# Performance work log

Measured on AMD Instinct MI355X. Metric: run time of the kernel, lower is better.

Reference implementation:

```python
import jax, jax.numpy as jnp
import numpy as np

EPS = 1e-5
SCALE = 2
K_UP = 5


def _conv(x, w, pad):
    return jax.lax.conv_general_dilated(
        x, w, window_strides=(1, 1), padding=[(pad, pad), (pad, pad)],
        dimension_numbers=("NCHW", "OIHW", "NCHW"))


def _bn(x, gamma, beta, mean, var):
    scale = gamma / jnp.sqrt(var + EPS)
    return x * scale[None, :, None, None] + (beta - mean * scale)[None, :, None, None]


def _pixel_shuffle(x, r):
    b, cr2, h, w = x.shape
    c = cr2 // (r * r)
    x = x.reshape(b, c, r, r, h, w)
    x = x.transpose(0, 1, 4, 2, 5, 3)  # b, c, h, r, w, r
    return x.reshape(b, c, h * r, w * r)


def setup_inputs() -> dict:
    key = jax.random.key(0)
    ks = jax.random.split(key, 6)
    c, c_mid, k_enc = 256, 64, 3
    n_k = (SCALE * K_UP) ** 2  # 100
    return {
        "x": jax.random.normal(ks[0], (2, c, 64, 64), jnp.float32),
        "comp_w": jax.random.normal(ks[1], (c_mid, c, 1, 1), jnp.float32) * 0.05,
        "comp_gamma": jnp.ones((c_mid,), jnp.float32),
        "comp_beta": jnp.zeros((c_mid,), jnp.float32),
        "comp_mean": jax.random.normal(ks[2], (c_mid,), jnp.float32) * 0.1,
        "comp_var": jax.random.uniform(ks[3], (c_mid,), jnp.float32, 0.5, 1.5),
        "enc_w": jax.random.normal(ks[4], (n_k, c_mid, k_enc, k_enc), jnp.float32) * 0.05,
        "enc_gamma": jnp.ones((n_k,), jnp.float32),
        "enc_beta": jnp.zeros((n_k,), jnp.float32),
        "enc_mean": jax.random.normal(ks[5], (n_k,), jnp.float32) * 0.1,
        "enc_var": jnp.ones((n_k,), jnp.float32),
    }


def reference(x, comp_w, comp_gamma, comp_beta, comp_mean, comp_var,
              enc_w, enc_gamma, enc_beta, enc_mean, enc_var):
    b, c, h, w = x.shape
    h_, w_ = h * SCALE, w * SCALE
    # comp: 1x1 conv -> BN -> ReLU
    W = jax.nn.relu(_bn(_conv(x, comp_w, 0), comp_gamma, comp_beta, comp_mean, comp_var))
    # enc: 3x3 conv -> BN (no relu)
    W = _bn(_conv(W, enc_w, 1), enc_gamma, enc_beta, enc_mean, enc_var)
    # pixel shuffle to [b, k_up^2, h_, w_] then softmax over kernel dim
    W = _pixel_shuffle(W, SCALE)
    W = jax.nn.softmax(W, axis=1)
    # nearest upsample x2
    Xu = jnp.repeat(jnp.repeat(x, SCALE, axis=2), SCALE, axis=3)
    # unfold: kernel k_up, dilation=SCALE, padding=k_up//2*SCALE
    pad = (K_UP // 2) * SCALE
    Xp = jnp.pad(Xu, ((0, 0), (0, 0), (pad, pad), (pad, pad)))
    patches = jnp.stack(
        [Xp[:, :, i * SCALE:i * SCALE + h_, j * SCALE:j * SCALE + w_]
         for i in range(K_UP) for j in range(K_UP)], axis=2)  # [b,c,k^2,h_,w_]
    return jnp.einsum("bkhw,bckhw->bchw", W, patches)
```

## Files before the change

### kernel.cpp

```cpp
#include <hip/hip_runtime.h>
#include <hip/hip_bf16.h>

#define EPSF 1e-5f

__global__ void k1_comp(const float* __restrict__ x, const float* __restrict__ w,
                        const float* __restrict__ gamma, const float* __restrict__ beta,
                        const float* __restrict__ mean, const float* __restrict__ var,
                        float* __restrict__ comp) {
    int t = blockIdx.x * 256 + threadIdx.x;
    int p  = t & 4095;
    int mq = (t >> 12) & 15;
    int b  = t >> 16;
    int m0 = mq * 4;
    const float* xb = x + b * (256 * 4096) + p;
    float acc[4] = {0.f, 0.f, 0.f, 0.f};
    #pragma unroll 16
    for (int c = 0; c < 256; ++c) {
        float xv = xb[c << 12];
        #pragma unroll
        for (int m = 0; m < 4; ++m)
            acc[m] += xv * w[(m0 + m) * 256 + c];
    }
    #pragma unroll
    for (int m = 0; m < 4; ++m) {
        int mo = m0 + m;
        float s = gamma[mo] * rsqrtf(var[mo] + EPSF);
        float r = acc[m] * s + (beta[mo] - mean[mo] * s);
        comp[(b * 64 + mo) * 4096 + p] = fmaxf(r, 0.f);
    }
}

__global__ void k2_enc_part(const float* __restrict__ comp, const float* __restrict__ w,
                            float* __restrict__ encp) {
    __shared__ float sh[16 * 18 * 18];
    const int tile = blockIdx.x;
    const int og   = blockIdx.y >> 2;
    const int icc  = blockIdx.y & 3;
    const int b    = blockIdx.z;
    const int ty0 = (tile >> 2) << 4;
    const int tx0 = (tile & 3) << 4;
    const int tid = threadIdx.x;
    const int tx = tid & 15, ty = tid >> 4;
    const int o0 = og * 10;

    const float* cb = comp + b * (64 * 4096);
    for (int idx = tid; idx < 16 * 324; idx += 256) {
        int ic_l = idx / 324;
        int rem  = idx - ic_l * 324;
        int yy = rem / 18;
        int xx = rem - yy * 18;
        int gy = ty0 + yy - 1;
        int gx = tx0 + xx - 1;
        float v = 0.f;
        if (gy >= 0 && gy < 64 && gx >= 0 && gx < 64)
            v = cb[((icc * 16 + ic_l) << 12) + (gy << 6) + gx];
        sh[idx] = v;
    }
    __syncthreads();

    float acc[10];
    #pragma unroll
    for (int i = 0; i < 10; ++i) acc[i] = 0.f;

    #pragma unroll 4
    for (int ic_l = 0; ic_l < 16; ++ic_l) {
        const float* base = sh + ic_l * 324 + ty * 18 + tx;
        float v[9];
        #pragma unroll
        for (int dy = 0; dy < 3; ++dy)
            #pragma unroll
            for (int dx = 0; dx < 3; ++dx)
                v[dy * 3 + dx] = base[dy * 18 + dx];
        const int ic = icc * 16 + ic_l;
        #pragma unroll
        for (int o_l = 0; o_l < 10; ++o_l) {
            const float* wp = w + ((o0 + o_l) * 64 + ic) * 9;
            #pragma unroll
            for (int q = 0; q < 9; ++q)
                acc[o_l] += wp[q] * v[q];
        }
    }
    const int pix = ((ty0 + ty) << 6) + tx0 + tx;
    #pragma unroll
    for (int o_l = 0; o_l < 10; ++o_l)
        encp[((icc * 2 + b) * 100 + o0 + o_l) * 4096 + pix] = acc[o_l];
}

__global__ void k3_softmax(const float* __restrict__ encp,
                           const float* __restrict__ gamma, const float* __restrict__ beta,
                           const float* __restrict__ mean, const float* __restrict__ var,
                           float* __restrict__ Wsm) {
    int t = blockIdx.x * 256 + threadIdx.x;
    int pos = t & 4095;
    int g   = (t >> 12) & 3;
    int b   = t >> 14;
    float v[25];
    float mx = -1e30f;
    #pragma unroll
    for (int k = 0; k < 25; ++k) {
        int o = k * 4 + g;
        float a = 0.f;
        #pragma unroll
        for (int icc = 0; icc < 4; ++icc)
            a += encp[((icc * 2 + b) * 100 + o) * 4096 + pos];
        float s = gamma[o] * rsqrtf(var[o] + EPSF);
        v[k] = a * s + (beta[o] - mean[o] * s);
        mx = fmaxf(mx, v[k]);
    }
    float s = 0.f;
    #pragma unroll
    for (int k = 0; k < 25; ++k) { v[k] = __expf(v[k] - mx); s += v[k]; }
    float inv = 1.f / s;
    float* o = Wsm + ((b * 4 + g) * 25) * 4096 + pos;
    #pragma unroll
    for (int k = 0; k < 25; ++k) o[k * 4096] = v[k] * inv;
}

__global__ void k4_gather(const float* __restrict__ x, const float* __restrict__ Wsm,
                          float* __restrict__ out) {
    __shared__ float4 patch[12 * 21];
    const int tile   = blockIdx.x;
    const int cchunk = blockIdx.y;
    const int b      = blockIdx.z;
    const int ly0 = (tile >> 2) << 3;
    const int lx0 = (tile & 3) << 4;
    const int tid = threadIdx.x;
    const int ph = tid >> 7;
    const int r  = tid & 127;
    const int ly = r >> 4, lx = r & 15;
    const int yl = ly0 + ly, xl = lx0 + lx;

    float w0[25], w1[25];
    {
        const float* wp0 = Wsm + ((b * 4 + ph * 2    ) * 25) * 4096 + yl * 64 + xl;
        const float* wp1 = Wsm + ((b * 4 + ph * 2 + 1) * 25) * 4096 + yl * 64 + xl;
        #pragma unroll
        for (int k = 0; k < 25; ++k) { w0[k] = wp0[k * 4096]; w1[k] = wp1[k * 4096]; }
    }
    const int pr = tid / 20, pc = tid % 20;
    const int gy = ly0 - 2 + pr, gx = lx0 - 2 + pc;
    const bool inb = (tid < 240) && (gy >= 0) && (gy < 64) && (gx >= 0) && (gx < 64);

    for (int cg = 0; cg < 4; ++cg) {
        const int c0 = cchunk * 16 + cg * 4;
        if (tid < 240) {
            float4 v = {0.f, 0.f, 0.f, 0.f};
            if (inb) {
                const float* xp = x + ((b * 256 + c0) * 4096) + gy * 64 + gx;
                v.x = xp[0]; v.y = xp[4096]; v.z = xp[8192]; v.w = xp[12288];
            }
            patch[pr * 21 + pc] = v;
        }
        __syncthreads();
        float4 a0 = {0.f, 0.f, 0.f, 0.f};
        float4 a1 = {0.f, 0.f, 0.f, 0.f};
        #pragma unroll
        for (int i = 0; i < 5; ++i) {
            #pragma unroll
            for (int j = 0; j < 5; ++j) {
                float4 xv = patch[(ly + i) * 21 + (lx + j)];
                float wa = w0[i * 5 + j], wb = w1[i * 5 + j];
                a0.x += wa * xv.x; a0.y += wa * xv.y; a0.z += wa * xv.z; a0.w += wa * xv.w;
                a1.x += wb * xv.x; a1.y += wb * xv.y; a1.z += wb * xv.z; a1.w += wb * xv.w;
            }
        }
        float* ob = out + (b * 256 + c0) * 16384 + (2 * yl + ph) * 128 + 2 * xl;
        float2 s0 = {a0.x, a1.x}; *(float2*)(ob)           = s0;
        float2 s1 = {a0.y, a1.y}; *(float2*)(ob + 16384)   = s1;
        float2 s2 = {a0.z, a1.z}; *(float2*)(ob + 32768)   = s2;
        float2 s3 = {a0.w, a1.w}; *(float2*)(ob + 49152)   = s3;
        __syncthreads();
    }
}

extern "C" void kernel_launch(void* const* d_in, const int* in_sizes, int n_in,
                              void* d_out, int out_size, void* d_ws, size_t ws_size,
                              hipStream_t stream) {
    const float* x          = (const float*)d_in[0];
    const float* comp_w     = (const float*)d_in[1];
    const float* comp_gamma = (const float*)d_in[2];
    const float* comp_beta  = (const float*)d_in[3];
    const float* comp_mean  = (const float*)d_in[4];
    const float* comp_var   = (const float*)d_in[5];
    const float* enc_w      = (const float*)d_in[6];
    const float* enc_gamma  = (const float*)d_in[7];
    const float* enc_beta   = (const float*)d_in[8];
    const float* enc_mean   = (const float*)d_in[9];
    const float* enc_var    = (const float*)d_in[10];
    float* out = (float*)d_out;

    float* ws   = (float*)d_ws;
    float* comp = ws;
    float* encp = ws + 524288;
    float* Wsm  = ws + 524288 + 3276800;

    k1_comp<<<dim3(512), dim3(256), 0, stream>>>(x, comp_w, comp_gamma, comp_beta,
                                                 comp_mean, comp_var, comp);
    k2_enc_part<<<dim3(16, 40, 2), dim3(256), 0, stream>>>(comp, enc_w, encp);
    k3_softmax<<<dim3(128), dim3(256), 0, stream>>>(encp, enc_gamma, enc_beta,
                                                    enc_mean, enc_var, Wsm);
    k4_gather<<<dim3(32, 16, 2), dim3(256), 0, stream>>>(x, Wsm, out);
}
```

Baseline: 157.9 us.

## Tile 1x1 conv with double-buffered shared-memory staging and store softmax weights in bf16

The 1x1 compression conv now has each block stage 32-channel slices of a 64-pixel tile in double-buffered shared memory, with each wave computing 8 output channels. This replaces the per-thread strided global loads and cuts redundant reads of x across output-channel groups. Separately, the softmax kernel writes its weights as bf16 and the gather kernel converts them back to float, halving that intermediate's traffic at some cost in precision of the blending weights.

```diff
diff --git a/kernel.cpp b/kernel.cpp
--- a/kernel.cpp
+++ b/kernel.cpp
@@ -1,32 +1,61 @@
 #include <hip/hip_runtime.h>
 #include <hip/hip_bf16.h>
 
+typedef __hip_bfloat16 bf16;
 #define EPSF 1e-5f
 
 __global__ void k1_comp(const float* __restrict__ x, const float* __restrict__ w,
                         const float* __restrict__ gamma, const float* __restrict__ beta,
                         const float* __restrict__ mean, const float* __restrict__ var,
                         float* __restrict__ comp) {
-    int t = blockIdx.x * 256 + threadIdx.x;
-    int p  = t & 4095;
-    int mq = (t >> 12) & 15;
-    int b  = t >> 16;
-    int m0 = mq * 4;
-    const float* xb = x + b * (256 * 4096) + p;
-    float acc[4] = {0.f, 0.f, 0.f, 0.f};
-    #pragma unroll 16
-    for (int c = 0; c < 256; ++c) {
-        float xv = xb[c << 12];
-        #pragma unroll
-        for (int m = 0; m < 4; ++m)
-            acc[m] += xv * w[(m0 + m) * 256 + c];
-    }
-    #pragma unroll
-    for (int m = 0; m < 4; ++m) {
-        int mo = m0 + m;
+    __shared__ float shx[2][32 * 64];
+    const int pxt = blockIdx.x;
+    const int ocg = blockIdx.y;
+    const int b   = blockIdx.z;
+    const int tid  = threadIdx.x;
+    const int wave = tid >> 6, lane = tid & 63;
+    const int oc0 = ocg * 32 + wave * 8;
+    const int px0 = pxt << 6;
+    const float* xb = x + b * (256 * 4096) + px0;
+
+    float acc[8] = {0.f, 0.f, 0.f, 0.f, 0.f, 0.f, 0.f, 0.f};
+
+    #pragma unroll
+    for (int i = 0; i < 2; ++i) {
+        int f4  = tid * 2 + i;
+        int row = f4 >> 4, col4 = f4 & 15;
+        float4 v = *(const float4*)(xb + row * 4096 + col4 * 4);
+        *(float4*)(&shx[0][row * 64 + col4 * 4]) = v;
+    }
+    __syncthreads();
+
+    for (int icc = 0; icc < 8; ++icc) {
+        const int buf = icc & 1;
+        if (icc < 7) {
+            #pragma unroll
+            for (int i = 0; i < 2; ++i) {
+                int f4  = tid * 2 + i;
+                int row = f4 >> 4, col4 = f4 & 15;
+                float4 v = *(const float4*)(xb + ((icc + 1) * 32 + row) * 4096 + col4 * 4);
+                *(float4*)(&shx[buf ^ 1][row * 64 + col4 * 4]) = v;
+            }
+        }
+        #pragma unroll 8
+        for (int ic_l = 0; ic_l < 32; ++ic_l) {
+            float xv = shx[buf][ic_l * 64 + lane];
+            const float* wp = w + icc * 32 + ic_l;
+            #pragma unroll
+            for (int m = 0; m < 8; ++m)
+                acc[m] += xv * wp[(oc0 + m) * 256];
+        }
+        __syncthreads();
+    }
+    #pragma unroll
+    for (int m = 0; m < 8; ++m) {
+        int mo = oc0 + m;
         float s = gamma[mo] * rsqrtf(var[mo] + EPSF);
         float r = acc[m] * s + (beta[mo] - mean[mo] * s);
-        comp[(b * 64 + mo) * 4096 + p] = fmaxf(r, 0.f);
+        comp[(b * 64 + mo) * 4096 + px0 + lane] = fmaxf(r, 0.f);
     }
 }
 
@@ -89,7 +118,7 @@
 __global__ void k3_softmax(const float* __restrict__ encp,
                            const float* __restrict__ gamma, const float* __restrict__ beta,
                            const float* __restrict__ mean, const float* __restrict__ var,
-                           float* __restrict__ Wsm) {
+                           bf16* __restrict__ Wsm) {
     int t = blockIdx.x * 256 + threadIdx.x;
     int pos = t & 4095;
     int g   = (t >> 12) & 3;
@@ -111,12 +140,12 @@
     #pragma unroll
     for (int k = 0; k < 25; ++k) { v[k] = __expf(v[k] - mx); s += v[k]; }
     float inv = 1.f / s;
-    float* o = Wsm + ((b * 4 + g) * 25) * 4096 + pos;
-    #pragma unroll
-    for (int k = 0; k < 25; ++k) o[k * 4096] = v[k] * inv;
-}
-
-__global__ void k4_gather(const float* __restrict__ x, const float* __restrict__ Wsm,
+    bf16* o = Wsm + ((b * 4 + g) * 25) * 4096 + pos;
+    #pragma unroll
+    for (int k = 0; k < 25; ++k) o[k * 4096] = __float2bfloat16(v[k] * inv);
+}
+
+__global__ void k4_gather(const float* __restrict__ x, const bf16* __restrict__ Wsm,
                           float* __restrict__ out) {
     __shared__ float4 patch[12 * 21];
     const int tile   = blockIdx.x;
@@ -132,10 +161,13 @@
 
     float w0[25], w1[25];
     {
-        const float* wp0 = Wsm + ((b * 4 + ph * 2    ) * 25) * 4096 + yl * 64 + xl;
-        const float* wp1 = Wsm + ((b * 4 + ph * 2 + 1) * 25) * 4096 + yl * 64 + xl;
-        #pragma unroll
-        for (int k = 0; k < 25; ++k) { w0[k] = wp0[k * 4096]; w1[k] = wp1[k * 4096]; }
+        const bf16* wp0 = Wsm + ((b * 4 + ph * 2    ) * 25) * 4096 + yl * 64 + xl;
+        const bf16* wp1 = Wsm + ((b * 4 + ph * 2 + 1) * 25) * 4096 + yl * 64 + xl;
+        #pragma unroll
+        for (int k = 0; k < 25; ++k) {
+            w0[k] = __bfloat162float(wp0[k * 4096]);
+            w1[k] = __bfloat162float(wp1[k * 4096]);
+        }
     }
     const int pr = tid / 20, pc = tid % 20;
     const int gy = ly0 - 2 + pr, gx = lx0 - 2 + pc;
@@ -192,10 +224,10 @@
     float* ws   = (float*)d_ws;
     float* comp = ws;
     float* encp = ws + 524288;
-    float* Wsm  = ws + 524288 + 3276800;
-
-    k1_comp<<<dim3(512), dim3(256), 0, stream>>>(x, comp_w, comp_gamma, comp_beta,
-                                                 comp_mean, comp_var, comp);
+    bf16*  Wsm  = (bf16*)(ws + 524288 + 3276800);
+
+    k1_comp<<<dim3(64, 2, 2), dim3(256), 0, stream>>>(x, comp_w, comp_gamma, comp_beta,
+                                                      comp_mean, comp_var, comp);
     k2_enc_part<<<dim3(16, 40, 2), dim3(256), 0, stream>>>(comp, enc_w, encp);
     k3_softmax<<<dim3(128), dim3(256), 0, stream>>>(encp, enc_gamma, enc_beta,
                                                     enc_mean, enc_var, Wsm);
```

Measured after the change: 157.1 us. Within noise of the previous version (-0.5%).
